# Performance work log

Measured on AMD Instinct MI355X. Metric: run time of the kernel, lower is better.

The kernel has to match this reference:

```python
import jax, jax.numpy as jnp
import numpy as np

V, E, C, H = 50000, 300, 128, 128
B, SC, SE = 128, 512, 64


def gru_scan(x, lengths, gate_w, gate_b, cand_w, cand_b):
    """TF GRUCell dynamic_rnn: x [B,S,E] -> outputs [B,S,C], zeroed past lengths."""
    Bn, S, _ = x.shape
    Cn = cand_w.shape[1]

    def step(h, inp):
        xt, t = inp  # xt [B,E]
        ru = jax.nn.sigmoid(jnp.concatenate([xt, h], axis=-1) @ gate_w + gate_b)
        r, u = jnp.split(ru, 2, axis=-1)
        c = jnp.tanh(jnp.concatenate([xt, r * h], axis=-1) @ cand_w + cand_b)
        hn = u * h + (1.0 - u) * c
        active = (t < lengths)[:, None]
        hn = jnp.where(active, hn, h)
        out = jnp.where(active, hn, 0.0)
        return hn, out

    h0 = jnp.zeros((Bn, Cn), dtype=x.dtype)
    _, outs = jax.lax.scan(step, h0, (jnp.swapaxes(x, 0, 1), jnp.arange(S)))
    return jnp.swapaxes(outs, 0, 1)


def reverse_seq(x, lengths):
    """tf.reverse_sequence along time for [B,S,D]."""
    S = x.shape[1]
    t = jnp.arange(S)[None, :]
    L = lengths[:, None]
    idx = jnp.where(t < L, L - 1 - t, t)
    return jnp.take_along_axis(x, idx[:, :, None], axis=1)


def attend(states, att_v, att_w, att_b):
    # states [B,S,C]
    scores = jnp.einsum('bsd,d->bs', jnp.tanh(jnp.einsum('bsc,cd->bsd', states, att_w) + att_b), att_v)
    w = jax.nn.softmax(scores, axis=1)
    return jnp.einsum('bsc,bs->bc', states, w)


def extract_features(seq, lengths, embeddings,
                     fw_gate_w, fw_gate_b, fw_cand_w, fw_cand_b,
                     bw_gate_w, bw_gate_b, bw_cand_w, bw_cand_b,
                     att_v, att_w, att_b):
    emb = embeddings[seq]  # [B,S,E]
    fw_states = gru_scan(emb, lengths, fw_gate_w, fw_gate_b, fw_cand_w, fw_cand_b)
    emb_rev = reverse_seq(emb, lengths)
    bw_out = gru_scan(emb_rev, lengths, bw_gate_w, bw_gate_b, bw_cand_w, bw_cand_b)
    bw_states = reverse_seq(bw_out, lengths)
    fw_c = attend(fw_states, att_v, att_w, att_b)
    bw_c = attend(bw_states, att_v, att_w, att_b)
    return jnp.concatenate([fw_c, bw_c], axis=1)


def setup_inputs() -> dict:
    key = jax.random.key(0)
    ks = jax.random.split(key, 20)
    s = 0.05
    context = jax.random.randint(ks[0], (B, SC), 0, V, dtype=jnp.int32)
    end = jax.random.randint(ks[1], (B, SE), 0, V, dtype=jnp.int32)
    context_length = jnp.clip(jax.random.randint(ks[2], (B,), 1, SC + 1), 1, SC).astype(jnp.int32)
    end_length = jnp.clip(jax.random.randint(ks[3], (B,), 1, SE + 1), 1, SE).astype(jnp.int32)
    return {
        'context': context, 'end': end,
        'context_length': context_length, 'end_length': end_length,
        'embeddings': jax.random.normal(ks[4], (V, E), jnp.float32) * s,
        'fw_gate_w': jax.random.normal(ks[5], (E + C, 2 * C), jnp.float32) * s,
        'fw_gate_b': jnp.ones((2 * C,), jnp.float32),
        'fw_cand_w': jax.random.normal(ks[6], (E + C, C), jnp.float32) * s,
        'fw_cand_b': jnp.zeros((C,), jnp.float32),
        'bw_gate_w': jax.random.normal(ks[7], (E + C, 2 * C), jnp.float32) * s,
        'bw_gate_b': jnp.ones((2 * C,), jnp.float32),
        'bw_cand_w': jax.random.normal(ks[8], (E + C, C), jnp.float32) * s,
        'bw_cand_b': jnp.zeros((C,), jnp.float32),
        'att_v': jax.random.normal(ks[9], (C,), jnp.float32) * s,
        'att_w': jax.random.normal(ks[10], (C, C), jnp.float32) * s,
        'att_b': jnp.zeros((C,), jnp.float32),
        'hid_w': jax.random.normal(ks[11], (4 * C, H), jnp.float32) * s,
        'hid_b': jnp.zeros((H,), jnp.float32),
        'out_w': jax.random.normal(ks[12], (H, 1), jnp.float32) * s,
        'out_b': jnp.zeros((1,), jnp.float32),
    }


def reference(context, end, context_length, end_length, embeddings,
              fw_gate_w, fw_gate_b, fw_cand_w, fw_cand_b,
              bw_gate_w, bw_gate_b, bw_cand_w, bw_cand_b,
              att_v, att_w, att_b, hid_w, hid_b, out_w, out_b):
    ctx_f = extract_features(context, context_length, embeddings,
                             fw_gate_w, fw_gate_b, fw_cand_w, fw_cand_b,
                             bw_gate_w, bw_gate_b, bw_cand_w, bw_cand_b,
                             att_v, att_w, att_b)
    end_f = extract_features(end, end_length, embeddings,
                             fw_gate_w, fw_gate_b, fw_cand_w, fw_cand_b,
                             bw_gate_w, bw_gate_b, bw_cand_w, bw_cand_b,
                             att_v, att_w, att_b)
    feats = jnp.concatenate([ctx_f, end_f], axis=1)  # [B, 4C]
    hidden = jax.nn.relu(feats @ hid_w + hid_b)
    logit = (hidden @ out_w + out_b)[:, 0]  # [B]
    return logit
```

## Files before the change

kernel.cpp:

```cpp
#include <hip/hip_runtime.h>
#include <cstdint>
#include <cmath>

static constexpr int V_  = 50000;
static constexpr int E_  = 300;
static constexpr int C_  = 128;
static constexpr int B_  = 128;
static constexpr int SC_ = 512;
static constexpr int SE_ = 64;
static constexpr int NCOL = 768;
static constexpr int KP  = 320;

static constexpr size_t OFF_PROJ  = 0;
static constexpr size_t SZ_PROJ   = (size_t)V_ * NCOL;
static constexpr size_t OFF_WXP   = OFF_PROJ + SZ_PROJ;
static constexpr size_t SZ_WXP    = (size_t)304 * NCOL;
static constexpr size_t OFF_UALL  = OFF_WXP + SZ_WXP;
static constexpr size_t SZ_UALL   = (size_t)C_ * NCOL;
static constexpr size_t OFF_BIAS  = OFF_UALL + SZ_UALL;
static constexpr size_t SZ_BIAS   = NCOL;
static constexpr size_t OFF_ST    = OFF_BIAS + SZ_BIAS;
static constexpr size_t SZ_ST_CTX = (size_t)B_ * SC_ * C_;
static constexpr size_t SZ_ST_END = (size_t)B_ * SE_ * C_;
static constexpr size_t SZ_ST     = 2*SZ_ST_CTX + 2*SZ_ST_END;
static constexpr size_t OFF_FEATS = OFF_ST + SZ_ST;
static constexpr size_t SZ_FEATS  = (size_t)B_ * 512;
static constexpr size_t OFF_BT    = OFF_FEATS + SZ_FEATS;

typedef __attribute__((ext_vector_type(8))) short bf16x8;
typedef __attribute__((ext_vector_type(4))) float f32x4;

static __device__ __forceinline__ unsigned short f2bf_rne(float f) {
  unsigned u = __float_as_uint(f);
  unsigned r = u + 0x7fffu + ((u >> 16) & 1u);
  return (unsigned short)(r >> 16);
}

static __device__ __forceinline__ void gload_lds16(const short* g, short* l) {
  __builtin_amdgcn_global_load_lds(
      (const __attribute__((address_space(1))) void*)g,
      (__attribute__((address_space(3))) void*)l, 16, 0, 0);
}

static __device__ __forceinline__ float fast_sigmoid(float x) {
  return __builtin_amdgcn_rcpf(1.f + __expf(-x));
}
static __device__ __forceinline__ float fast_tanh(float x) {
  return fmaf(-2.f, __builtin_amdgcn_rcpf(__expf(2.f * x) + 1.f), 1.f);
}

__global__ void pack_kernel(const float* __restrict__ fw_gw, const float* __restrict__ fw_gb,
                            const float* __restrict__ fw_cw, const float* __restrict__ fw_cb,
                            const float* __restrict__ bw_gw, const float* __restrict__ bw_gb,
                            const float* __restrict__ bw_cw, const float* __restrict__ bw_cb,
                            float* __restrict__ ws) {
  int i = blockIdx.x * 256 + threadIdx.x;
  float* Wxp  = ws + OFF_WXP;
  float* Uall = ws + OFF_UALL;
  float* bias = ws + OFF_BIAS;
  if (i < 304 * NCOL) {
    int k = i / NCOL, c = i % NCOL;
    float v = 0.f;
    if (k < 300) {
      if (c < 256)      v = fw_gw[k*256 + c];
      else if (c < 384) v = fw_cw[k*128 + (c-256)];
      else if (c < 640) v = bw_gw[k*256 + (c-384)];
      else              v = bw_cw[k*128 + (c-640)];
    }
    Wxp[i] = v;
    return;
  }
  int j = i - 304 * NCOL;
  if (j >= 0 && j < 128 * NCOL) {
    int k = j / NCOL, c = j % NCOL;
    int kk = 300 + k;
    float v;
    if (c < 256)      v = fw_gw[kk*256 + c];
    else if (c < 384) v = fw_cw[kk*128 + (c-256)];
    else if (c < 640) v = bw_gw[kk*256 + (c-384)];
    else              v = bw_cw[kk*128 + (c-640)];
    Uall[j] = v;
    return;
  }
  int m = j - 128 * NCOL;
  if (m >= 0 && m < NCOL) {
    float v;
    if (m < 256)      v = fw_gb[m];
    else if (m < 384) v = fw_cb[m-256];
    else if (m < 640) v = bw_gb[m-384];
    else              v = bw_cb[m-640];
    bias[m] = v;
  }
}

__global__ void pack_bt(const float* __restrict__ Wxp, short* __restrict__ Bthi,
                        short* __restrict__ Btlo) {
  int i = blockIdx.x * 256 + threadIdx.x;
  if (i >= NCOL * KP) return;
  int k = i % KP, n = i / KP;
  float v = (k < 304) ? Wxp[(size_t)k * NCOL + n] : 0.f;
  unsigned short h = f2bf_rne(v);
  float hf = __uint_as_float((unsigned)h << 16);
  unsigned short lo = f2bf_rne(v - hf);
  Bthi[i] = (short)h;
  Btlo[i] = (short)lo;
}

__global__ void pack_emb(const float* __restrict__ emb, short* __restrict__ Ahi,
                         short* __restrict__ Alo) {
  size_t i = (size_t)blockIdx.x * 256 + threadIdx.x;
  if (i >= (size_t)V_ * KP) return;
  int k = (int)(i % KP);
  size_t row = i / KP;
  float v = (k < E_) ? emb[row * E_ + k] : 0.f;
  unsigned short h = f2bf_rne(v);
  float hf = __uint_as_float((unsigned)h << 16);
  unsigned short lo = f2bf_rne(v - hf);
  Ahi[i] = (short)h;
  Alo[i] = (short)lo;
}

__global__ __launch_bounds__(256) void gemm_mfma(
    const short* __restrict__ Ahi, const short* __restrict__ Alo,
    const short* __restrict__ Bthi, const short* __restrict__ Btlo,
    float* __restrict__ proj) {
  __shared__ short lds[16384];
  int tid = threadIdx.x, wid = tid >> 6, lane = tid & 63;
  int n0 = blockIdx.x * 128, m0 = blockIdx.y * 128;
  f32x4 acc[4][4] = {};

  int lr = lane >> 2, lc = lane & 3;
  int q0 = wid * 2, q1 = q0 + 1;
  int r0 = q0 * 16 + lr, r1 = q1 * 16 + lr;
  int am0 = m0 + r0; if (am0 > V_ - 1) am0 = V_ - 1;
  int am1 = m0 + r1; if (am1 > V_ - 1) am1 = V_ - 1;
  size_t gaOff0 = (size_t)am0 * KP + lc * 8;
  size_t gaOff1 = (size_t)am1 * KP + lc * 8;
  size_t gbOff0 = (size_t)(n0 + r0) * KP + lc * 8;
  size_t gbOff1 = (size_t)(n0 + r1) * KP + lc * 8;

  int quad = lane >> 4;
  int arow = (wid >> 1) * 64 + (lane & 15);
  int brow = (wid & 1) * 64 + (lane & 15);

  for (int k0 = 0; k0 < KP; k0 += 32) {
    gload_lds16(Ahi  + gaOff0 + k0, lds +         q0 * 512);
    gload_lds16(Ahi  + gaOff1 + k0, lds +         q1 * 512);
    gload_lds16(Alo  + gaOff0 + k0, lds +  4096 + q0 * 512);
    gload_lds16(Alo  + gaOff1 + k0, lds +  4096 + q1 * 512);
    gload_lds16(Bthi + gbOff0 + k0, lds +  8192 + q0 * 512);
    gload_lds16(Bthi + gbOff1 + k0, lds +  8192 + q1 * 512);
    gload_lds16(Btlo + gbOff0 + k0, lds + 12288 + q0 * 512);
    gload_lds16(Btlo + gbOff1 + k0, lds + 12288 + q1 * 512);
    __syncthreads();

    bf16x8 ah[4], al[4], bh[4], bl[4];
#pragma unroll
    for (int i = 0; i < 4; ++i) {
      ah[i] = *(bf16x8*)&lds[        (arow + i*16) * 32 + quad * 8];
      al[i] = *(bf16x8*)&lds[ 4096 + (arow + i*16) * 32 + quad * 8];
      bh[i] = *(bf16x8*)&lds[ 8192 + (brow + i*16) * 32 + quad * 8];
      bl[i] = *(bf16x8*)&lds[12288 + (brow + i*16) * 32 + quad * 8];
    }
#pragma unroll
    for (int i = 0; i < 4; ++i)
#pragma unroll
      for (int j = 0; j < 4; ++j) {
        acc[i][j] = __builtin_amdgcn_mfma_f32_16x16x32_bf16(ah[i], bh[j], acc[i][j], 0, 0, 0);
        acc[i][j] = __builtin_amdgcn_mfma_f32_16x16x32_bf16(ah[i], bl[j], acc[i][j], 0, 0, 0);
        acc[i][j] = __builtin_amdgcn_mfma_f32_16x16x32_bf16(al[i], bh[j], acc[i][j], 0, 0, 0);
      }
    __syncthreads();
  }

  int colb = n0 + (wid & 1) * 64 + (lane & 15);
  int rowb = m0 + (wid >> 1) * 64 + quad * 4;
#pragma unroll
  for (int i = 0; i < 4; ++i) {
    int rb = rowb + i * 16;
#pragma unroll
    for (int j = 0; j < 4; ++j) {
      int cc = colb + j * 16;
#pragma unroll
      for (int r = 0; r < 4; ++r) {
        int rr = rb + r;
        if (rr < V_) proj[(size_t)rr * NCOL + cc] = acc[i][j][r];
      }
    }
  }
}

__global__ __attribute__((amdgpu_flat_work_group_size(256, 256),
                          amdgpu_waves_per_eu(2, 2)))
void recur_kernel(
    const int* __restrict__ ctx, const int* __restrict__ endseq,
    const int* __restrict__ ctx_len, const int* __restrict__ end_len,
    const float* __restrict__ proj, const float* __restrict__ Uall,
    const float* __restrict__ bias, float* __restrict__ states) {
  __shared__ __align__(16) float h_s[128];
  __shared__ __align__(16) float rh_s[128];
  __shared__ __align__(16) float u_s[128];
  __shared__ __align__(16) float pg[8][260];
  __shared__ __align__(16) float pc[8][132];

  int bid = blockIdx.x;
  int tid = threadIdx.x;
  const int* seq; int S, L, b, dir; float* stbase;
  if (bid < 256) {
    b = bid >> 1; dir = bid & 1;
    seq = ctx + b * SC_; S = SC_; L = ctx_len[b];
    stbase = states + (dir ? SZ_ST_CTX : 0) + (size_t)b * SC_ * C_;
  } else {
    int q = bid - 256; b = q >> 1; dir = q & 1;
    seq = endseq + b * SE_; S = SE_; L = end_len[b];
    stbase = states + 2*SZ_ST_CTX + (dir ? SZ_ST_END : 0) + (size_t)b * SE_ * C_;
  }
  int dirOff = dir ? 384 : 0;
  int kg = tid >> 5, jg = tid & 31;

  float wg[16][8];
  float wc[16][4];
#pragma unroll
  for (int kk = 0; kk < 16; ++kk) {
    const float* up = Uall + (size_t)(kg*16 + kk) * NCOL + dirOff;
    float4 w0 = *(const float4*)(up + jg*8);
    float4 w1 = *(const float4*)(up + jg*8 + 4);
    wg[kk][0]=w0.x; wg[kk][1]=w0.y; wg[kk][2]=w0.z; wg[kk][3]=w0.w;
    wg[kk][4]=w1.x; wg[kk][5]=w1.y; wg[kk][6]=w1.z; wg[kk][7]=w1.w;
    float4 wv = *(const float4*)(up + 256 + jg*4);
    wc[kk][0]=wv.x; wc[kk][1]=wv.y; wc[kk][2]=wv.z; wc[kk][3]=wv.w;
  }
  float bias_g = bias[dirOff + tid];
  float bias_c = (tid < 128) ? bias[dirOff + 256 + tid] : 0.f;

  if (tid < 128) h_s[tid] = 0.f;
  __syncthreads();

  int pos0 = dir ? (L - 1) : 0;
  int tok0 = seq[pos0];
  const float* xr0 = proj + (size_t)tok0 * NCOL + dirOff;
  float xg = xr0[tid];
  float xc = (tid < 128) ? xr0[256 + tid] : 0.f;

  for (int t = 0; t < L; ++t) {
    float xg_n = 0.f, xc_n = 0.f;
    if (t + 1 < L) {
      int pos_n = dir ? (L - 2 - t) : (t + 1);
      int tok_n = seq[pos_n];
      const float* xr = proj + (size_t)tok_n * NCOL + dirOff;
      xg_n = xr[tid];
      xc_n = (tid < 128) ? xr[256 + tid] : 0.f;
    }

    float a[8] = {0.f,0.f,0.f,0.f,0.f,0.f,0.f,0.f};
    const float4* h4 = (const float4*)h_s;
#pragma unroll
    for (int q = 0; q < 4; ++q) {
      float4 hv = h4[kg*4 + q];
      float he[4] = {hv.x, hv.y, hv.z, hv.w};
#pragma unroll
      for (int e = 0; e < 4; ++e)
#pragma unroll
        for (int jj = 0; jj < 8; ++jj)
          a[jj] += he[e] * wg[q*4 + e][jj];
    }
    *(float4*)(&pg[kg][jg*8])     = make_float4(a[0], a[1], a[2], a[3]);
    *(float4*)(&pg[kg][jg*8 + 4]) = make_float4(a[4], a[5], a[6], a[7]);
    __syncthreads();

    float g = xg + bias_g;
#pragma unroll
    for (int k2 = 0; k2 < 8; ++k2) g += pg[k2][tid];
    g = fast_sigmoid(g);

    float h_old = 0.f;
    if (tid < 128) { h_old = h_s[tid]; rh_s[tid] = g * h_old; }
    else           { u_s[tid - 128] = g; }
    __syncthreads();

    float ac[4] = {0.f, 0.f, 0.f, 0.f};
    const float4* rh4 = (const float4*)rh_s;
#pragma unroll
    for (int q = 0; q < 4; ++q) {
      float4 rv = rh4[kg*4 + q];
      float re[4] = {rv.x, rv.y, rv.z, rv.w};
#pragma unroll
      for (int e = 0; e < 4; ++e)
#pragma unroll
        for (int jj = 0; jj < 4; ++jj)
          ac[jj] += re[e] * wc[q*4 + e][jj];
    }
    *(float4*)(&pc[kg][jg*4]) = make_float4(ac[0], ac[1], ac[2], ac[3]);
    __syncthreads();

    if (tid < 128) {
      float cs = xc + bias_c;
#pragma unroll
      for (int k2 = 0; k2 < 8; ++k2) cs += pc[k2][tid];
      float c = fast_tanh(cs);
      float u = u_s[tid];
      float hn = u * h_old + (1.f - u) * c;
      h_s[tid] = hn;
      int pos = dir ? (L - 1 - t) : t;
      stbase[(size_t)pos * C_ + tid] = hn;
    }
    __syncthreads();
    xg = xg_n; xc = xc_n;
  }

  for (int i = L * C_ + tid; i < S * C_; i += 256) stbase[i] = 0.f;
}

__global__ __launch_bounds__(256, 2) void attn_kernel(
    const float* __restrict__ states, const float* __restrict__ att_v,
    const float* __restrict__ att_w, const float* __restrict__ att_b,
    float* __restrict__ feats) {
  __shared__ __align__(16) float st_s[8][132];
  __shared__ __align__(16) float pgA[8][8][132];
  __shared__ float score_s[8];
  __shared__ float cm[128], cl[128], ca[128];

  int bid = blockIdx.x, tid = threadIdx.x;
  int b, dir, S, featOff; const float* stb;
  if (bid < 256) {
    b = bid >> 1; dir = bid & 1; S = SC_;
    stb = states + (dir ? SZ_ST_CTX : 0) + (size_t)b * SC_ * C_;
    featOff = dir * 128;
  } else {
    int q = bid - 256; b = q >> 1; dir = q & 1; S = SE_;
    stb = states + 2*SZ_ST_CTX + (dir ? SZ_ST_END : 0) + (size_t)b * SE_ * C_;
    featOff = 256 + dir * 128;
  }

  int kg = tid >> 5, jg = tid & 31;
  float wreg[16][4];
#pragma unroll
  for (int kk = 0; kk < 16; ++kk) {
    float4 wv = *(const float4*)(att_w + (size_t)(kg*16 + kk) * C_ + jg*4);
    wreg[kk][0]=wv.x; wreg[kk][1]=wv.y; wreg[kk][2]=wv.z; wreg[kk][3]=wv.w;
  }
  int d0 = jg * 4;
  float4 b4 = *(const float4*)(att_b + d0);
  float4 v4 = *(const float4*)(att_v + d0);
  int c = tid & 127, half = tid >> 7;

  float m = -1e30f, lsum = 0.f, acc = 0.f;

  for (int s0 = 0; s0 < S; s0 += 8) {
    __syncthreads();
    for (int lId = tid; lId < 1024; lId += 256) {
      int r = lId >> 7, k = lId & 127;
      st_s[r][k] = stb[(size_t)(s0 + r) * C_ + k];
    }
    __syncthreads();

    float pacc[8][4] = {};
#pragma unroll
    for (int r = 0; r < 8; ++r) {
      const float4* srow4 = (const float4*)(&st_s[r][0]);
#pragma unroll
      for (int q = 0; q < 4; ++q) {
        float4 sv = srow4[kg*4 + q];
        float se[4] = {sv.x, sv.y, sv.z, sv.w};
#pragma unroll
        for (int e = 0; e < 4; ++e)
#pragma unroll
          for (int jj = 0; jj < 4; ++jj)
            pacc[r][jj] += se[e] * wreg[q*4 + e][jj];
      }
    }
#pragma unroll
    for (int r = 0; r < 8; ++r)
      *(float4*)(&pgA[kg][r][jg*4]) =
          make_float4(pacc[r][0], pacc[r][1], pacc[r][2], pacc[r][3]);
    __syncthreads();

    float4 p4 = make_float4(0.f, 0.f, 0.f, 0.f);
#pragma unroll
    for (int k2 = 0; k2 < 8; ++k2) {
      float4 t4 = *(const float4*)(&pgA[k2][kg][d0]);
      p4.x += t4.x; p4.y += t4.y; p4.z += t4.z; p4.w += t4.w;
    }
    float sc = tanhf(p4.x + b4.x) * v4.x + tanhf(p4.y + b4.y) * v4.y +
               tanhf(p4.z + b4.z) * v4.z + tanhf(p4.w + b4.w) * v4.w;
#pragma unroll
    for (int off = 16; off > 0; off >>= 1) sc += __shfl_xor(sc, off, 64);
    if (jg == 0) score_s[kg] = sc;
    __syncthreads();

    float srow[8]; float smax = m;
#pragma unroll
    for (int r = 0; r < 8; ++r) { srow[r] = score_s[r]; smax = fmaxf(smax, srow[r]); }
    float scale = expf(m - smax);
    acc *= scale; lsum *= scale; m = smax;
#pragma unroll
    for (int rr = 0; rr < 4; ++rr) {
      int r = half * 4 + rr;
      float w = expf(srow[r] - m);
      lsum += w;
      acc += w * st_s[r][c];
    }
  }

  __syncthreads();
  if (half == 1) { cm[c] = m; cl[c] = lsum; ca[c] = acc; }
  __syncthreads();
  if (half == 0) {
    float m1 = cm[c], l1 = cl[c], a1 = ca[c];
    float M = fmaxf(m, m1);
    float w0 = expf(m - M), w1 = expf(m1 - M);
    feats[b * 512 + featOff + c] = (acc * w0 + a1 * w1) / (lsum * w0 + l1 * w1);
  }
}

__global__ __launch_bounds__(128) void head_kernel(
    const float* __restrict__ feats, const float* __restrict__ hid_w,
    const float* __restrict__ hid_b, const float* __restrict__ out_w,
    const float* __restrict__ out_b, float* __restrict__ out) {
  __shared__ __align__(16) float f_s[512];
  __shared__ float part[2];
  int b = blockIdx.x, tid = threadIdx.x;
  for (int i = tid; i < 512; i += 128) f_s[i] = feats[b * 512 + i];
  __syncthreads();
  float h = hid_b[tid];
  for (int k = 0; k < 512; ++k) h += f_s[k] * hid_w[k * 128 + tid];
  h = fmaxf(h, 0.f);
  float p = h * out_w[tid];
#pragma unroll
  for (int off = 32; off > 0; off >>= 1) p += __shfl_xor(p, off, 64);
  if ((tid & 63) == 0) part[tid >> 6] = p;
  __syncthreads();
  if (tid == 0) out[b] = part[0] + part[1] + out_b[0];
}

extern "C" void kernel_launch(void* const* d_in, const int* in_sizes, int n_in,
                              void* d_out, int out_size, void* d_ws, size_t ws_size,
                              hipStream_t stream) {
  const int*   ctx     = (const int*)d_in[0];
  const int*   endseq  = (const int*)d_in[1];
  const int*   ctx_len = (const int*)d_in[2];
  const int*   end_len = (const int*)d_in[3];
  const float* emb     = (const float*)d_in[4];
  const float* fw_gw   = (const float*)d_in[5];
  const float* fw_gb   = (const float*)d_in[6];
  const float* fw_cw   = (const float*)d_in[7];
  const float* fw_cb   = (const float*)d_in[8];
  const float* bw_gw   = (const float*)d_in[9];
  const float* bw_gb   = (const float*)d_in[10];
  const float* bw_cw   = (const float*)d_in[11];
  const float* bw_cb   = (const float*)d_in[12];
  const float* att_v   = (const float*)d_in[13];
  const float* att_w   = (const float*)d_in[14];
  const float* att_b   = (const float*)d_in[15];
  const float* hid_w   = (const float*)d_in[16];
  const float* hid_b   = (const float*)d_in[17];
  const float* out_w   = (const float*)d_in[18];
  const float* out_b   = (const float*)d_in[19];
  float* ws  = (float*)d_ws;
  float* out = (float*)d_out;

  short* Ahi  = (short*)(ws + OFF_ST);
  short* Alo  = Ahi + (size_t)V_ * KP;
  short* Bthi = (short*)(ws + OFF_BT);
  short* Btlo = Bthi + (size_t)NCOL * KP;

  pack_kernel<<<1299, 256, 0, stream>>>(fw_gw, fw_gb, fw_cw, fw_cb,
                                        bw_gw, bw_gb, bw_cw, bw_cb, ws);
  pack_bt<<<(NCOL * KP + 255) / 256, 256, 0, stream>>>(ws + OFF_WXP, Bthi, Btlo);
  pack_emb<<<(int)(((size_t)V_ * KP + 255) / 256), 256, 0, stream>>>(emb, Ahi, Alo);

  dim3 ggrid(6, 391);
  gemm_mfma<<<ggrid, 256, 0, stream>>>(Ahi, Alo, Bthi, Btlo, ws + OFF_PROJ);

  recur_kernel<<<512, 256, 0, stream>>>(ctx, endseq, ctx_len, end_len,
                                        ws + OFF_PROJ, ws + OFF_UALL,
                                        ws + OFF_BIAS, ws + OFF_ST);

  attn_kernel<<<512, 256, 0, stream>>>(ws + OFF_ST, att_v, att_w, att_b,
                                       ws + OFF_FEATS);

  head_kernel<<<128, 128, 0, stream>>>(ws + OFF_FEATS, hid_w, hid_b,
                                       out_w, out_b, out);
}
```

Measured before the change: 910.0 us.

## Restructure GRU recurrence to 512 threads with register-resident hidden state and shuffles

The recurrence kernel moves from 256 to 512 threads per block. Each wave now owns 16 hidden units held in registers and broadcasts them with wave shuffles instead of going through shared memory. This removes the h/rh/u shared buffers and two of the four block barriers per time step, cutting the sequential per-step latency. The cost is more threads per block, a different cross-wave reduction layout, and a heavier reliance on shuffle throughput; per-thread weight registers are halved.

```diff
diff --git a/kernel.cpp b/kernel.cpp
--- a/kernel.cpp
+++ b/kernel.cpp
@@ -190,17 +190,14 @@
   }
 }
 
-__global__ __attribute__((amdgpu_flat_work_group_size(256, 256),
-                          amdgpu_waves_per_eu(2, 2)))
+__global__ __attribute__((amdgpu_flat_work_group_size(512, 512),
+                          amdgpu_waves_per_eu(4, 4)))
 void recur_kernel(
     const int* __restrict__ ctx, const int* __restrict__ endseq,
     const int* __restrict__ ctx_len, const int* __restrict__ end_len,
     const float* __restrict__ proj, const float* __restrict__ Uall,
     const float* __restrict__ bias, float* __restrict__ states) {
-  __shared__ __align__(16) float h_s[128];
-  __shared__ __align__(16) float rh_s[128];
-  __shared__ __align__(16) float u_s[128];
-  __shared__ __align__(16) float pg[8][260];
+  __shared__ __align__(16) float pg[8][288];
   __shared__ __align__(16) float pc[8][132];
 
   int bid = blockIdx.x;
@@ -216,99 +213,86 @@
     stbase = states + 2*SZ_ST_CTX + (dir ? SZ_ST_END : 0) + (size_t)b * SE_ * C_;
   }
   int dirOff = dir ? 384 : 0;
-  int kg = tid >> 5, jg = tid & 31;
-
-  float wg[16][8];
-  float wc[16][4];
+  int w = tid >> 6, lane = tid & 63;
+  int l15 = lane & 15;
+  int hidx  = 16 * w + l15;
+  int gcol4 = 4 * lane;
+  int pgidx = (lane < 32) ? 4 * lane : 4 * lane + 16;
+  int ccol2 = 2 * lane;
+  bool is_r = ((lane & 31) < 16);
+  int scol  = is_r ? (16 * w + l15) : (128 + 16 * w + l15);
+  int sidx  = is_r ? (16 * w + l15) : (144 + 16 * w + l15);
+
+  float wgt[16][4];
+  float wct[16][2];
 #pragma unroll
   for (int kk = 0; kk < 16; ++kk) {
-    const float* up = Uall + (size_t)(kg*16 + kk) * NCOL + dirOff;
-    float4 w0 = *(const float4*)(up + jg*8);
-    float4 w1 = *(const float4*)(up + jg*8 + 4);
-    wg[kk][0]=w0.x; wg[kk][1]=w0.y; wg[kk][2]=w0.z; wg[kk][3]=w0.w;
-    wg[kk][4]=w1.x; wg[kk][5]=w1.y; wg[kk][6]=w1.z; wg[kk][7]=w1.w;
-    float4 wv = *(const float4*)(up + 256 + jg*4);
-    wc[kk][0]=wv.x; wc[kk][1]=wv.y; wc[kk][2]=wv.z; wc[kk][3]=wv.w;
-  }
-  float bias_g = bias[dirOff + tid];
-  float bias_c = (tid < 128) ? bias[dirOff + 256 + tid] : 0.f;
-
-  if (tid < 128) h_s[tid] = 0.f;
-  __syncthreads();
+    const float* up = Uall + (size_t)(16 * w + kk) * NCOL + dirOff;
+    float4 g4 = *(const float4*)(up + gcol4);
+    wgt[kk][0] = g4.x; wgt[kk][1] = g4.y; wgt[kk][2] = g4.z; wgt[kk][3] = g4.w;
+    float2 c2 = *(const float2*)(up + 256 + ccol2);
+    wct[kk][0] = c2.x; wct[kk][1] = c2.y;
+  }
+  float bias_g = bias[dirOff + scol];
+  float bias_c = bias[dirOff + 256 + hidx];
+
+  float h = 0.f;
 
   int pos0 = dir ? (L - 1) : 0;
-  int tok0 = seq[pos0];
-  const float* xr0 = proj + (size_t)tok0 * NCOL + dirOff;
-  float xg = xr0[tid];
-  float xc = (tid < 128) ? xr0[256 + tid] : 0.f;
+  const float* xr0 = proj + (size_t)seq[pos0] * NCOL + dirOff;
+  float xg = xr0[scol];
+  float xc = xr0[256 + hidx];
 
   for (int t = 0; t < L; ++t) {
     float xg_n = 0.f, xc_n = 0.f;
     if (t + 1 < L) {
       int pos_n = dir ? (L - 2 - t) : (t + 1);
-      int tok_n = seq[pos_n];
-      const float* xr = proj + (size_t)tok_n * NCOL + dirOff;
-      xg_n = xr[tid];
-      xc_n = (tid < 128) ? xr[256 + tid] : 0.f;
-    }
-
-    float a[8] = {0.f,0.f,0.f,0.f,0.f,0.f,0.f,0.f};
-    const float4* h4 = (const float4*)h_s;
-#pragma unroll
-    for (int q = 0; q < 4; ++q) {
-      float4 hv = h4[kg*4 + q];
-      float he[4] = {hv.x, hv.y, hv.z, hv.w};
-#pragma unroll
-      for (int e = 0; e < 4; ++e)
-#pragma unroll
-        for (int jj = 0; jj < 8; ++jj)
-          a[jj] += he[e] * wg[q*4 + e][jj];
-    }
-    *(float4*)(&pg[kg][jg*8])     = make_float4(a[0], a[1], a[2], a[3]);
-    *(float4*)(&pg[kg][jg*8 + 4]) = make_float4(a[4], a[5], a[6], a[7]);
+      const float* xr = proj + (size_t)seq[pos_n] * NCOL + dirOff;
+      xg_n = xr[scol];
+      xc_n = xr[256 + hidx];
+    }
+
+    float a0 = 0.f, a1 = 0.f, a2 = 0.f, a3 = 0.f;
+#pragma unroll
+    for (int k = 0; k < 16; ++k) {
+      float hk = __shfl(h, k, 64);
+      a0 += hk * wgt[k][0]; a1 += hk * wgt[k][1];
+      a2 += hk * wgt[k][2]; a3 += hk * wgt[k][3];
+    }
+    *(float4*)(&pg[w][pgidx]) = make_float4(a0, a1, a2, a3);
     __syncthreads();
 
     float g = xg + bias_g;
 #pragma unroll
-    for (int k2 = 0; k2 < 8; ++k2) g += pg[k2][tid];
+    for (int w2 = 0; w2 < 8; ++w2) g += pg[w2][sidx];
     g = fast_sigmoid(g);
 
-    float h_old = 0.f;
-    if (tid < 128) { h_old = h_s[tid]; rh_s[tid] = g * h_old; }
-    else           { u_s[tid - 128] = g; }
-    __syncthreads();
-
-    float ac[4] = {0.f, 0.f, 0.f, 0.f};
-    const float4* rh4 = (const float4*)rh_s;
-#pragma unroll
-    for (int q = 0; q < 4; ++q) {
-      float4 rv = rh4[kg*4 + q];
-      float re[4] = {rv.x, rv.y, rv.z, rv.w};
-#pragma unroll
-      for (int e = 0; e < 4; ++e)
-#pragma unroll
-        for (int jj = 0; jj < 4; ++jj)
-          ac[jj] += re[e] * wc[q*4 + e][jj];
-    }
-    *(float4*)(&pc[kg][jg*4]) = make_float4(ac[0], ac[1], ac[2], ac[3]);
-    __syncthreads();
-
-    if (tid < 128) {
-      float cs = xc + bias_c;
-#pragma unroll
-      for (int k2 = 0; k2 < 8; ++k2) cs += pc[k2][tid];
-      float c = fast_tanh(cs);
-      float u = u_s[tid];
-      float hn = u * h_old + (1.f - u) * c;
-      h_s[tid] = hn;
+    float rh = g * h;
+
+    float c0 = 0.f, c1 = 0.f;
+#pragma unroll
+    for (int k = 0; k < 16; ++k) {
+      float rhk = __shfl(rh, k, 64);
+      c0 += rhk * wct[k][0]; c1 += rhk * wct[k][1];
+    }
+    *(float2*)(&pc[w][ccol2]) = make_float2(c0, c1);
+    __syncthreads();
+
+    float cs = xc + bias_c;
+#pragma unroll
+    for (int w2 = 0; w2 < 8; ++w2) cs += pc[w2][hidx];
+    float c = fast_tanh(cs);
+    float u = __shfl(g, 16 + l15, 64);
+    float hn = u * h + (1.f - u) * c;
+    h = hn;
+    if (lane < 16) {
       int pos = dir ? (L - 1 - t) : t;
-      stbase[(size_t)pos * C_ + tid] = hn;
-    }
-    __syncthreads();
+      stbase[(size_t)pos * C_ + hidx] = hn;
+    }
     xg = xg_n; xc = xc_n;
   }
 
-  for (int i = L * C_ + tid; i < S * C_; i += 256) stbase[i] = 0.f;
+  for (int i = L * C_ + tid; i < S * C_; i += 512) stbase[i] = 0.f;
 }
 
 __global__ __launch_bounds__(256, 2) void attn_kernel(
@@ -472,7 +456,7 @@
   dim3 ggrid(6, 391);
   gemm_mfma<<<ggrid, 256, 0, stream>>>(Ahi, Alo, Bthi, Btlo, ws + OFF_PROJ);
 
-  recur_kernel<<<512, 256, 0, stream>>>(ctx, endseq, ctx_len, end_len,
+  recur_kernel<<<512, 512, 0, stream>>>(ctx, endseq, ctx_len, end_len,
                                         ws + OFF_PROJ, ws + OFF_UALL,
                                         ws + OFF_BIAS, ws + OFF_ST);
 
```

After: 1.597 ms. 1.75x slower.

## Move attention projection onto split-bf16 MFMA with register-prefetched state chunks

Applied to the files above, without the earlier changes.

Rewrites the attention kernel so the states×att_w projection uses 16x16x32 bf16 MFMA with a hi/lo split (three products) in place of scalar FP32 FMAs plus a cross-group LDS reduction. att_w is pre-split into transposed bf16 hi/lo arrays in the existing pack_bt launch. Chunks grow from 8 to 16 rows, the next chunk is prefetched into registers, and expf/tanhf are replaced with fast intrinsics. This aims to cut ALU and LDS traffic in the attention stage, at the cost of slightly reduced projection precision and extra conversion work per chunk.

```diff
diff --git a/kernel.cpp b/kernel.cpp
--- a/kernel.cpp
+++ b/kernel.cpp
@@ -26,6 +26,8 @@
 static constexpr size_t OFF_FEATS = OFF_ST + SZ_ST;
 static constexpr size_t SZ_FEATS  = (size_t)B_ * 512;
 static constexpr size_t OFF_BT    = OFF_FEATS + SZ_FEATS;
+static constexpr size_t SZ_BT     = (size_t)NCOL * KP / 2 * 2;
+static constexpr size_t OFF_AWT   = OFF_BT + SZ_BT;
 
 typedef __attribute__((ext_vector_type(8))) short bf16x8;
 typedef __attribute__((ext_vector_type(4))) float f32x4;
@@ -94,16 +96,29 @@
 }
 
 __global__ void pack_bt(const float* __restrict__ Wxp, short* __restrict__ Bthi,
-                        short* __restrict__ Btlo) {
+                        short* __restrict__ Btlo, const float* __restrict__ att_w,
+                        short* __restrict__ awt_hi, short* __restrict__ awt_lo) {
   int i = blockIdx.x * 256 + threadIdx.x;
-  if (i >= NCOL * KP) return;
-  int k = i % KP, n = i / KP;
-  float v = (k < 304) ? Wxp[(size_t)k * NCOL + n] : 0.f;
-  unsigned short h = f2bf_rne(v);
-  float hf = __uint_as_float((unsigned)h << 16);
-  unsigned short lo = f2bf_rne(v - hf);
-  Bthi[i] = (short)h;
-  Btlo[i] = (short)lo;
+  if (i < NCOL * KP) {
+    int k = i % KP, n = i / KP;
+    float v = (k < 304) ? Wxp[(size_t)k * NCOL + n] : 0.f;
+    unsigned short h = f2bf_rne(v);
+    float hf = __uint_as_float((unsigned)h << 16);
+    unsigned short lo = f2bf_rne(v - hf);
+    Bthi[i] = (short)h;
+    Btlo[i] = (short)lo;
+    return;
+  }
+  int j = i - NCOL * KP;
+  if (j < 128 * 128) {
+    int d = j >> 7, c = j & 127;
+    float v = att_w[(size_t)c * 128 + d];
+    unsigned short h = f2bf_rne(v);
+    float hf = __uint_as_float((unsigned)h << 16);
+    unsigned short lo = f2bf_rne(v - hf);
+    awt_hi[j] = (short)h;
+    awt_lo[j] = (short)lo;
+  }
 }
 
 __global__ void pack_emb(const float* __restrict__ emb, short* __restrict__ Ahi,
@@ -312,12 +327,14 @@
 }
 
 __global__ __launch_bounds__(256, 2) void attn_kernel(
-    const float* __restrict__ states, const float* __restrict__ att_v,
-    const float* __restrict__ att_w, const float* __restrict__ att_b,
-    float* __restrict__ feats) {
-  __shared__ __align__(16) float st_s[8][132];
-  __shared__ __align__(16) float pgA[8][8][132];
-  __shared__ float score_s[8];
+    const float* __restrict__ states, const short* __restrict__ awt_hi,
+    const short* __restrict__ awt_lo, const float* __restrict__ att_v,
+    const float* __restrict__ att_b, float* __restrict__ feats) {
+  __shared__ __align__(16) float st_s[16][132];
+  __shared__ __align__(16) short ah_s[16][132];
+  __shared__ __align__(16) short al_s[16][132];
+  __shared__ float spart[4][16];
+  __shared__ float score_s[16];
   __shared__ float cm[128], cl[128], ca[128];
 
   int bid = blockIdx.x, tid = threadIdx.x;
@@ -332,73 +349,96 @@
     featOff = 256 + dir * 128;
   }
 
-  int kg = tid >> 5, jg = tid & 31;
-  float wreg[16][4];
-#pragma unroll
-  for (int kk = 0; kk < 16; ++kk) {
-    float4 wv = *(const float4*)(att_w + (size_t)(kg*16 + kk) * C_ + jg*4);
-    wreg[kk][0]=wv.x; wreg[kk][1]=wv.y; wreg[kk][2]=wv.z; wreg[kk][3]=wv.w;
-  }
-  int d0 = jg * 4;
-  float4 b4 = *(const float4*)(att_b + d0);
-  float4 v4 = *(const float4*)(att_v + d0);
+  int w = tid >> 6, lane = tid & 63;
+  int quad = lane >> 4, l15 = lane & 15;
+
+  int d0 = 32 * w + l15, d1 = d0 + 16;
+  bf16x8 bh0[4], bh1[4], bl0[4], bl1[4];
+#pragma unroll
+  for (int kt = 0; kt < 4; ++kt) {
+    bh0[kt] = *(const bf16x8*)&awt_hi[d0*128 + kt*32 + quad*8];
+    bh1[kt] = *(const bf16x8*)&awt_hi[d1*128 + kt*32 + quad*8];
+    bl0[kt] = *(const bf16x8*)&awt_lo[d0*128 + kt*32 + quad*8];
+    bl1[kt] = *(const bf16x8*)&awt_lo[d1*128 + kt*32 + quad*8];
+  }
+  float vv0 = att_v[d0], vv1 = att_v[d1];
+  float bb0 = att_b[d0], bb1 = att_b[d1];
+
   int c = tid & 127, half = tid >> 7;
-
   float m = -1e30f, lsum = 0.f, acc = 0.f;
 
-  for (int s0 = 0; s0 < S; s0 += 8) {
-    __syncthreads();
-    for (int lId = tid; lId < 1024; lId += 256) {
-      int r = lId >> 7, k = lId & 127;
-      st_s[r][k] = stb[(size_t)(s0 + r) * C_ + k];
-    }
-    __syncthreads();
-
-    float pacc[8][4] = {};
+  int lrow = tid >> 4, lcol = (tid & 15) * 8;
+  float4 p0, p1;
+  {
+    const float* src = stb + (size_t)lrow * C_ + lcol;
+    p0 = *(const float4*)(src);
+    p1 = *(const float4*)(src + 4);
+  }
+
+  int nchunks = S >> 4;
+  for (int ch = 0; ch < nchunks; ++ch) {
+    __syncthreads();
+    float f[8] = {p0.x, p0.y, p0.z, p0.w, p1.x, p1.y, p1.z, p1.w};
+    short hi8[8], lo8[8];
+#pragma unroll
+    for (int j = 0; j < 8; ++j) {
+      unsigned short h = f2bf_rne(f[j]);
+      float hf = __uint_as_float((unsigned)h << 16);
+      hi8[j] = (short)h;
+      lo8[j] = (short)f2bf_rne(f[j] - hf);
+    }
+    *(float4*)(&st_s[lrow][lcol])     = p0;
+    *(float4*)(&st_s[lrow][lcol + 4]) = p1;
+    *(bf16x8*)(&ah_s[lrow][lcol]) = *(bf16x8*)hi8;
+    *(bf16x8*)(&al_s[lrow][lcol]) = *(bf16x8*)lo8;
+    if (ch + 1 < nchunks) {
+      const float* src = stb + (size_t)((ch + 1) * 16 + lrow) * C_ + lcol;
+      p0 = *(const float4*)(src);
+      p1 = *(const float4*)(src + 4);
+    }
+    __syncthreads();
+
+    f32x4 ac0 = {0.f, 0.f, 0.f, 0.f}, ac1 = {0.f, 0.f, 0.f, 0.f};
+#pragma unroll
+    for (int kt = 0; kt < 4; ++kt) {
+      bf16x8 a_hi = *(bf16x8*)&ah_s[l15][kt*32 + quad*8];
+      bf16x8 a_lo = *(bf16x8*)&al_s[l15][kt*32 + quad*8];
+      ac0 = __builtin_amdgcn_mfma_f32_16x16x32_bf16(a_hi, bh0[kt], ac0, 0, 0, 0);
+      ac0 = __builtin_amdgcn_mfma_f32_16x16x32_bf16(a_hi, bl0[kt], ac0, 0, 0, 0);
+      ac0 = __builtin_amdgcn_mfma_f32_16x16x32_bf16(a_lo, bh0[kt], ac0, 0, 0, 0);
+      ac1 = __builtin_amdgcn_mfma_f32_16x16x32_bf16(a_hi, bh1[kt], ac1, 0, 0, 0);
+      ac1 = __builtin_amdgcn_mfma_f32_16x16x32_bf16(a_hi, bl1[kt], ac1, 0, 0, 0);
+      ac1 = __builtin_amdgcn_mfma_f32_16x16x32_bf16(a_lo, bh1[kt], ac1, 0, 0, 0);
+    }
+
+    float part[4];
+#pragma unroll
+    for (int r = 0; r < 4; ++r)
+      part[r] = fast_tanh(ac0[r] + bb0) * vv0 + fast_tanh(ac1[r] + bb1) * vv1;
+#pragma unroll
+    for (int mask = 1; mask <= 8; mask <<= 1)
+#pragma unroll
+      for (int r = 0; r < 4; ++r)
+        part[r] += __shfl_xor(part[r], mask, 64);
+    if (l15 == 0) {
+#pragma unroll
+      for (int r = 0; r < 4; ++r) spart[w][quad*4 + r] = part[r];
+    }
+    __syncthreads();
+    if (tid < 16)
+      score_s[tid] = spart[0][tid] + spart[1][tid] + spart[2][tid] + spart[3][tid];
+    __syncthreads();
+
+    float srow[8]; float smax = m;
+#pragma unroll
+    for (int r = 0; r < 8; ++r) { srow[r] = score_s[half*8 + r]; smax = fmaxf(smax, srow[r]); }
+    float scale = __expf(m - smax);
+    acc *= scale; lsum *= scale; m = smax;
 #pragma unroll
     for (int r = 0; r < 8; ++r) {
-      const float4* srow4 = (const float4*)(&st_s[r][0]);
-#pragma unroll
-      for (int q = 0; q < 4; ++q) {
-        float4 sv = srow4[kg*4 + q];
-        float se[4] = {sv.x, sv.y, sv.z, sv.w};
-#pragma unroll
-        for (int e = 0; e < 4; ++e)
-#pragma unroll
-          for (int jj = 0; jj < 4; ++jj)
-            pacc[r][jj] += se[e] * wreg[q*4 + e][jj];
-      }
-    }
-#pragma unroll
-    for (int r = 0; r < 8; ++r)
-      *(float4*)(&pgA[kg][r][jg*4]) =
-          make_float4(pacc[r][0], pacc[r][1], pacc[r][2], pacc[r][3]);
-    __syncthreads();
-
-    float4 p4 = make_float4(0.f, 0.f, 0.f, 0.f);
-#pragma unroll
-    for (int k2 = 0; k2 < 8; ++k2) {
-      float4 t4 = *(const float4*)(&pgA[k2][kg][d0]);
-      p4.x += t4.x; p4.y += t4.y; p4.z += t4.z; p4.w += t4.w;
-    }
-    float sc = tanhf(p4.x + b4.x) * v4.x + tanhf(p4.y + b4.y) * v4.y +
-               tanhf(p4.z + b4.z) * v4.z + tanhf(p4.w + b4.w) * v4.w;
-#pragma unroll
-    for (int off = 16; off > 0; off >>= 1) sc += __shfl_xor(sc, off, 64);
-    if (jg == 0) score_s[kg] = sc;
-    __syncthreads();
-
-    float srow[8]; float smax = m;
-#pragma unroll
-    for (int r = 0; r < 8; ++r) { srow[r] = score_s[r]; smax = fmaxf(smax, srow[r]); }
-    float scale = expf(m - smax);
-    acc *= scale; lsum *= scale; m = smax;
-#pragma unroll
-    for (int rr = 0; rr < 4; ++rr) {
-      int r = half * 4 + rr;
-      float w = expf(srow[r] - m);
-      lsum += w;
-      acc += w * st_s[r][c];
+      float wgt = __expf(srow[r] - m);
+      lsum += wgt;
+      acc += wgt * st_s[half*8 + r][c];
     }
   }
 
@@ -408,7 +448,7 @@
   if (half == 0) {
     float m1 = cm[c], l1 = cl[c], a1 = ca[c];
     float M = fmaxf(m, m1);
-    float w0 = expf(m - M), w1 = expf(m1 - M);
+    float w0 = __expf(m - M), w1 = __expf(m1 - M);
     feats[b * 512 + featOff + c] = (acc * w0 + a1 * w1) / (lsum * w0 + l1 * w1);
   }
 }
@@ -459,14 +499,17 @@
   float* ws  = (float*)d_ws;
   float* out = (float*)d_out;
 
-  short* Ahi  = (short*)(ws + OFF_ST);
-  short* Alo  = Ahi + (size_t)V_ * KP;
-  short* Bthi = (short*)(ws + OFF_BT);
-  short* Btlo = Bthi + (size_t)NCOL * KP;
+  short* Ahi    = (short*)(ws + OFF_ST);
+  short* Alo    = Ahi + (size_t)V_ * KP;
+  short* Bthi   = (short*)(ws + OFF_BT);
+  short* Btlo   = Bthi + (size_t)NCOL * KP;
+  short* awt_hi = (short*)(ws + OFF_AWT);
+  short* awt_lo = awt_hi + 128 * 128;
 
   pack_kernel<<<1299, 256, 0, stream>>>(fw_gw, fw_gb, fw_cw, fw_cb,
                                         bw_gw, bw_gb, bw_cw, bw_cb, ws);
-  pack_bt<<<(NCOL * KP + 255) / 256, 256, 0, stream>>>(ws + OFF_WXP, Bthi, Btlo);
+  pack_bt<<<(NCOL * KP + 128 * 128 + 255) / 256, 256, 0, stream>>>(
+      ws + OFF_WXP, Bthi, Btlo, att_w, awt_hi, awt_lo);
   pack_emb<<<(int)(((size_t)V_ * KP + 255) / 256), 256, 0, stream>>>(emb, Ahi, Alo);
 
   dim3 ggrid(6, 391);
@@ -476,8 +519,8 @@
                                         ws + OFF_PROJ, ws + OFF_UALL,
                                         ws + OFF_BIAS, ws + OFF_ST);
 
-  attn_kernel<<<512, 256, 0, stream>>>(ws + OFF_ST, att_v, att_w, att_b,
-                                       ws + OFF_FEATS);
+  attn_kernel<<<512, 256, 0, stream>>>(ws + OFF_ST, awt_hi, awt_lo,
+                                       att_v, att_b, ws + OFF_FEATS);
 
   head_kernel<<<128, 128, 0, stream>>>(ws + OFF_FEATS, hid_w, hid_b,
                                        out_w, out_b, out);
```

Result: faster. 764.4 us (-16.0%).
